# Kernel tuning notes

Hardware: AMD Instinct MI355X
Metric: run time of the kernel (lower is better)

Reference implementation:

```python
import jax, jax.numpy as jnp
import numpy as np

FRAME_LEN = 400
HOP = 160
FFT_LEN = 512
PREEMPH = 0.97
MEL_FLOOR = 1.192092955078125e-07


def _hertz_to_mel(freq):
    return 1127.0 * np.log(1.0 + freq / 700.0)


def _mel_filter_bank(num_frequency_bins=256, num_mel_filters=80, min_frequency=20.0,
                     max_frequency=8000.0, sampling_rate=16000):
    mel_min = _hertz_to_mel(min_frequency)
    mel_max = _hertz_to_mel(max_frequency)
    mel_freqs = np.linspace(mel_min, mel_max, num_mel_filters + 2)
    # NOTE: source has filter_freqs = mel_freqs (mel-space, intentional replication of bug)
    filter_freqs = mel_freqs
    fft_bin_width = sampling_rate / (num_frequency_bins * 2)
    fft_freqs = _hertz_to_mel(fft_bin_width * np.arange(num_frequency_bins))
    filter_diff = np.diff(filter_freqs)
    slopes = filter_freqs[None, :] - fft_freqs[:, None]          # [256, 82]
    down_slopes = -slopes[:, :-2] / filter_diff[:-1]
    up_slopes = slopes[:, 2:] / filter_diff[1:]
    fb = np.maximum(0.0, np.minimum(down_slopes, up_slopes))      # [256, 80]
    # F.pad(mel_filters, (0,0,0,1)) -> one extra zero row -> [257, 80]
    return np.pad(fb, ((0, 1), (0, 0))).astype(np.float32)


def _window():
    n = np.arange(FRAME_LEN)
    hann = 0.5 - 0.5 * np.cos(2.0 * np.pi * n / (FRAME_LEN - 1))  # periodic=False
    return (hann ** 0.85).astype(np.float32)


def setup_inputs() -> dict:
    key = jax.random.key(0)
    T = 9_600_000  # 10 min @ 16 kHz
    raw_speech = jax.random.normal(key, (1, T), dtype=jnp.float32)
    return {
        "raw_speech": raw_speech,
        "mel_filters": jnp.asarray(_mel_filter_bank()),  # [257, 80]
        "window": jnp.asarray(_window()),                # [400]
    }


def reference(raw_speech, mel_filters, window):
    wav = raw_speech.reshape(-1) * 32768.0  # * 2**15
    num_frames = 1 + (wav.shape[0] - FRAME_LEN) // HOP
    idx = jnp.arange(num_frames)[:, None] * HOP + jnp.arange(FRAME_LEN)[None, :]
    frames = wav[idx]                                         # [F, 400]
    frames = frames - frames.mean(axis=1, keepdims=True)      # remove DC offset
    # preemphasis: y[0] = x[0]*(1-p), y[n] = x[n] - p*x[n-1]
    pre = jnp.concatenate(
        [frames[:, :1] * (1.0 - PREEMPH), frames[:, 1:] - PREEMPH * frames[:, :-1]],
        axis=1,
    )
    pre = pre * window
    padded = jnp.pad(pre, ((0, 0), (0, FFT_LEN - FRAME_LEN)))  # [F, 512]
    spec = jnp.abs(jnp.fft.rfft(padded, axis=1)) ** 2          # [F, 257]
    mel = jnp.log(jnp.maximum(spec @ mel_filters, MEL_FLOOR))  # [F, 80]
    mean = mel.mean(axis=0, keepdims=True)
    var = mel.var(axis=0, keepdims=True, ddof=1)               # unbiased
    return (mel - mean) / jnp.sqrt(var + 1e-7)
```

## Files before the change

kernel.cpp:

```cpp
#include <hip/hip_runtime.h>
#include <math.h>

#define FRAME_LEN 400
#define HOP 160
#define NMEL 80
#define PREEMPH 0.97f
#define MEL_FLOOR 1.192092955078125e-07f
#define PPW 4
#define NSHADOW 8

#ifndef __has_builtin
#define __has_builtin(x) 0
#endif
#if __has_builtin(__builtin_amdgcn_permlane16_swap) && __has_builtin(__builtin_amdgcn_permlane32_swap)
#define USE_PLSWAP 1
#else
#define USE_PLSWAP 0
#endif
#if __has_builtin(__builtin_amdgcn_global_load_lds)
#define USE_GLL 1
typedef __attribute__((address_space(3))) void* as3_void_ptr;
typedef const __attribute__((address_space(1))) void* as1_void_cptr;
#define GLOAD_LDS(gsrc, ldst) \
    __builtin_amdgcn_global_load_lds((as1_void_cptr)(gsrc), (as3_void_ptr)(ldst), 16, 0, 0)
#else
#define USE_GLL 0
#endif

__device__ __forceinline__ float2 cadd(float2 a, float2 b){ return make_float2(a.x+b.x, a.y+b.y); }
__device__ __forceinline__ float2 csub(float2 a, float2 b){ return make_float2(a.x-b.x, a.y-b.y); }
__device__ __forceinline__ float2 cmul(float2 a, float2 b){ return make_float2(a.x*b.x-a.y*b.y, a.x*b.y+a.y*b.x); }

__device__ __forceinline__ float bperm(int addr, float v) {
    return __int_as_float(__builtin_amdgcn_ds_bpermute(addr, __float_as_int(v)));
}
template<int C>
__device__ __forceinline__ float dppf(float v) {
    return __int_as_float(__builtin_amdgcn_update_dpp(0, __float_as_int(v), C, 0xF, 0xF, false));
}
__device__ __forceinline__ float wscan_add(float v) {
    v += __int_as_float(__builtin_amdgcn_update_dpp(0, __float_as_int(v), 0x111, 0xF, 0xF, false));
    v += __int_as_float(__builtin_amdgcn_update_dpp(0, __float_as_int(v), 0x112, 0xF, 0xF, false));
    v += __int_as_float(__builtin_amdgcn_update_dpp(0, __float_as_int(v), 0x114, 0xF, 0xF, false));
    v += __int_as_float(__builtin_amdgcn_update_dpp(0, __float_as_int(v), 0x118, 0xF, 0xF, false));
    v += __int_as_float(__builtin_amdgcn_update_dpp(0, __float_as_int(v), 0x142, 0xA, 0xF, false));
    v += __int_as_float(__builtin_amdgcn_update_dpp(0, __float_as_int(v), 0x143, 0xC, 0xF, false));
    return v;
}

#if USE_PLSWAP
typedef unsigned int uint2v __attribute__((ext_vector_type(2)));
__device__ __forceinline__ void bflytw16(float2& A, float2& B, float2 tw) {
    uint2v sx = __builtin_amdgcn_permlane16_swap(__float_as_uint(A.x), __float_as_uint(B.x), false, false);
    uint2v sy = __builtin_amdgcn_permlane16_swap(__float_as_uint(A.y), __float_as_uint(B.y), false, false);
    float lx = __uint_as_float(sx.x), hx = __uint_as_float(sx.y);
    float ly = __uint_as_float(sy.x), hy = __uint_as_float(sy.y);
    float cr = tw.x * hx - tw.y * hy;
    float ci = tw.x * hy + tw.y * hx;
    float r1x = lx + cr, r2x = lx - cr;
    float r1y = ly + ci, r2y = ly - ci;
    uint2v tx = __builtin_amdgcn_permlane16_swap(__float_as_uint(r1x), __float_as_uint(r2x), false, false);
    uint2v ty = __builtin_amdgcn_permlane16_swap(__float_as_uint(r1y), __float_as_uint(r2y), false, false);
    A = make_float2(__uint_as_float(tx.x), __uint_as_float(ty.x));
    B = make_float2(__uint_as_float(tx.y), __uint_as_float(ty.y));
}
__device__ __forceinline__ void bflytw32(float2& A, float2& B, float2 tw) {
    uint2v sx = __builtin_amdgcn_permlane32_swap(__float_as_uint(A.x), __float_as_uint(B.x), false, false);
    uint2v sy = __builtin_amdgcn_permlane32_swap(__float_as_uint(A.y), __float_as_uint(B.y), false, false);
    float lx = __uint_as_float(sx.x), hx = __uint_as_float(sx.y);
    float ly = __uint_as_float(sy.x), hy = __uint_as_float(sy.y);
    float cr = tw.x * hx - tw.y * hy;
    float ci = tw.x * hy + tw.y * hx;
    float r1x = lx + cr, r2x = lx - cr;
    float r1y = ly + ci, r2y = ly - ci;
    uint2v tx = __builtin_amdgcn_permlane32_swap(__float_as_uint(r1x), __float_as_uint(r2x), false, false);
    uint2v ty = __builtin_amdgcn_permlane32_swap(__float_as_uint(r1y), __float_as_uint(r2y), false, false);
    A = make_float2(__uint_as_float(tx.x), __uint_as_float(ty.x));
    B = make_float2(__uint_as_float(tx.y), __uint_as_float(ty.y));
}
#endif

__global__ __launch_bounds__(256) void setup_kernel(const float* __restrict__ window,
                                                    float* __restrict__ frtab,
                                                    int* __restrict__ kstab,
                                                    float* __restrict__ wftab,
                                                    float* __restrict__ twtab)
{
    const int bid = blockIdx.x;
    const int t = threadIdx.x;
    if (bid == 0) {
        __shared__ float uu[256];
        const double mel_min = 1127.0 * log(1.0 + 20.0 / 700.0);
        const double mel_max = 1127.0 * log(1.0 + 8000.0 / 700.0);
        const double dstep = (mel_max - mel_min) / 81.0;
        {
            double fhz = 31.25 * (double)t;
            double m = 1127.0 * log(1.0 + fhz / 700.0);
            uu[t] = (float)((m - mel_min) / dstep);
        }
        __syncthreads();
        {
            float u = uu[t];
            frtab[t] = u - floorf(u);
        }
        if (t < 82) {
            double fhz = 700.0 * (exp((mel_min + (double)t * dstep) / 1127.0) - 1.0);
            int k = (int)ceil(fhz / 31.25);
            k = max(0, min(256, k));
            while (k > 0 && uu[k - 1] >= (float)t) --k;
            while (k < 256 && uu[k] < (float)t) ++k;
            kstab[t] = k;
        }
        if (t < 64) {
            const int l = t;
            const int bl = __brev((unsigned)l) >> 26;
            float* o = twtab + 24 * l;
            #pragma unroll
            for (int j = 1; j <= 3; ++j) {
                int d = 1 << j;
                float2 tw = make_float2(1.f, 0.f);
                if (l & d) {
                    float tt = (float)(l & (d - 1));
                    float ang = -3.1415926535897932f * tt / (float)d;
                    sincosf(ang, &tw.y, &tw.x);
                }
                o[2 * (j - 1)]     = tw.x;
                o[2 * (j - 1) + 1] = tw.y;
            }
            {
                float a16 = -3.1415926535897932f * (float)(l & 15) * (1.0f / 16.0f);
                float a32 = -3.1415926535897932f * (float)(l & 31) * (1.0f / 32.0f);
                float s16, c16, s32, c32;
                sincosf(a16, &s16, &c16);
                sincosf(a32, &s32, &c32);
                o[6] = c16; o[7] = s16; o[8] = c32; o[9] = s32;
            }
            #pragma unroll
            for (int q = 1; q < 4; ++q) {
                float ang = -6.283185307179586f * (float)(bl * q) * (1.0f / 256.0f);
                float sv, cv;
                sincosf(ang, &sv, &cv);
                o[8 + 2 * q] = cv; o[9 + 2 * q] = sv;
            }
            #pragma unroll
            for (int q = 0; q < 4; ++q) {
                int k = 4 * l + q;
                float ang = -3.1415926535897932f * (float)k * (1.0f / 256.0f);
                float sv, cv;
                sincosf(ang, &sv, &cv);
                o[16 + 2 * q] = cv; o[17 + 2 * q] = sv;
            }
        }
    } else {
        if (t >= 64) return;
        const int k = bid - 1;
        float sr = 0.f, si = 0.f;
        #pragma unroll
        for (int j = 0; j < 7; ++j) {
            int n = t + 64 * j;
            if (n < FRAME_LEN) {
                float wv = window[n] * 32768.f;
                int m = (k * n) & 511;
                float ang = -3.1415926535897932f * (float)m * (1.0f / 256.0f);
                float sv, cv;
                sincosf(ang, &sv, &cv);
                sr = fmaf(wv, cv, sr);
                si = fmaf(wv, sv, si);
            }
        }
        sr = wscan_add(sr);
        si = wscan_add(si);
        if (t == 63) { wftab[2 * k] = sr; wftab[2 * k + 1] = si; }
    }
}

__global__ __launch_bounds__(64, 8) void feat_kernel(
    const float* __restrict__ raw, const float* __restrict__ window,
    float* __restrict__ mel_out, double* __restrict__ accum,
    const float* __restrict__ frtab, const int* __restrict__ kstab,
    const float* __restrict__ wftab, const float* __restrict__ twtab, int F)
{
    __shared__ __align__(16) float wlds[FRAME_LEN];
    __shared__ __align__(16) float xu[2][560];
    __shared__ __align__(16) float pfx[2][256];

    const int l = threadIdx.x;
    const int NP = (F + 1) >> 1;
    const int basePair = blockIdx.x * PPW;

    if (basePair < NP) {
        int fA0 = 2 * basePair;
        bool hasB0 = (fA0 + 1) < F;
        const float* g = raw + (size_t)fA0 * HOP;
#if USE_GLL
        GLOAD_LDS(g + 4 * l, xu[0]);
        if (hasB0 || l < 36) GLOAD_LDS(g + 256 + 4 * l, xu[0] + 256);
        if (hasB0 && l < 12) GLOAD_LDS(g + 512 + 4 * l, xu[0] + 512);
#else
        float4 a = ((const float4*)g)[l];
        float4 b = make_float4(0.f,0.f,0.f,0.f);
        float4 c = make_float4(0.f,0.f,0.f,0.f);
        if (hasB0 || l < 36) b = ((const float4*)g)[64 + l];
        if (hasB0 && l < 12) c = ((const float4*)g)[128 + l];
        ((float4*)xu[0])[l] = a;
        ((float4*)xu[0])[64 + l] = b;
        if (l < 12) ((float4*)xu[0])[128 + l] = c;
#endif
    }

    for (int i = l; i < FRAME_LEN; i += 64) wlds[i] = window[i] * 32768.f;

    const int bl   = __brev((unsigned)l) >> 26;
    const int adrX = (l ^ 63) << 2;
    const int adr0 = ((64 - l) & 63) << 2;

    float sg[4];
    #pragma unroll
    for (int j = 0; j < 4; ++j) sg[j] = (l & (1 << j)) ? -1.f : 1.f;

    float2 dt[3], tw16, tw32, w2[4], wk[4];
    {
        const float2* tl = (const float2*)(twtab + 24 * l);
        dt[0] = tl[0];
        dt[1] = tl[1];
        dt[2] = tl[2];
        tw16  = tl[3];
        tw32  = tl[4];
        w2[1] = tl[5];
        w2[2] = tl[6];
        w2[3] = tl[7];
        wk[0] = tl[8];
        wk[1] = tl[9];
        wk[2] = tl[10];
        wk[3] = tl[11];
    }
#if !USE_PLSWAP
    float2 dtf[2];
    float sgf[2];
    #pragma unroll
    for (int j = 4; j <= 5; ++j) {
        int d = 1 << j;
        sgf[j - 4] = (l & d) ? -1.f : 1.f;
        float2 tw = make_float2(1.f, 0.f);
        if (l & d) {
            float tt = (float)(l & (d - 1));
            float ang = -3.1415926535897932f * tt / (float)d;
            sincosf(ang, &tw.y, &tw.x);
        }
        dtf[j - 4] = tw;
    }
#endif

    float wfr[4], wfi[4];
    {
        const float2* wf2 = (const float2*)wftab;
        float2 w0 = wf2[4 * l], w1 = wf2[4 * l + 1], w2v = wf2[4 * l + 2], w3 = wf2[4 * l + 3];
        wfr[0] = w0.x; wfi[0] = w0.y; wfr[1] = w1.x; wfi[1] = w1.y;
        wfr[2] = w2v.x; wfi[2] = w2v.y; wfr[3] = w3.x; wfi[3] = w3.y;
    }

    float fr1[4];
    {
        float4 fv = *(const float4*)(frtab + 4 * l);
        fr1[0] = fv.x; fr1[1] = fv.y; fr1[2] = fv.z; fr1[3] = fv.w;
    }
    int a0 = kstab[l], b0 = kstab[l + 1], e0 = kstab[l + 2];
    int a1 = 1, b1 = 1, e1 = 1;
    if (l < 16) { a1 = kstab[64 + l]; b1 = kstab[65 + l]; e1 = kstab[66 + l]; }

    float acc_s0 = 0.f, acc_q0 = 0.f;
    float acc_s1 = 0.f, acc_q1 = 0.f;

    int  fPrev = -1;
    bool hasBPrev = false;
    float vA0 = 0.f, vA1 = 0.f, vB0 = 0.f, vB1 = 0.f;

    for (int fi = 0; fi < PPW; ++fi) {
        int P = basePair + fi;
        if (P >= NP) break;
        int fA = 2 * P;
        bool hasB = (fA + 1) < F;
        const int cur = fi & 1;

        asm volatile("s_waitcnt vmcnt(0)" ::: "memory");

        const bool ldn = (fi + 1 < PPW) && (P + 1 < NP);
        if (ldn) {
            int fAn = 2 * (P + 1);
            bool hasBn = (fAn + 1) < F;
            const float* g = raw + (size_t)fAn * HOP;
            float* xn = xu[cur ^ 1];
#if USE_GLL
            GLOAD_LDS(g + 4 * l, xn);
            if (hasBn || l < 36) GLOAD_LDS(g + 256 + 4 * l, xn + 256);
            if (hasBn && l < 12) GLOAD_LDS(g + 512 + 4 * l, xn + 512);
#else
            float4 a = ((const float4*)g)[l];
            float4 b = make_float4(0.f,0.f,0.f,0.f);
            float4 c = make_float4(0.f,0.f,0.f,0.f);
            if (hasBn || l < 36) b = ((const float4*)g)[64 + l];
            if (hasBn && l < 12) c = ((const float4*)g)[128 + l];
            ((float4*)xn)[l] = a;
            ((float4*)xn)[64 + l] = b;
            if (l < 12) ((float4*)xn)[128 + l] = c;
#endif
        }

        if (fPrev >= 0) {
            mel_out[(size_t)fPrev * NMEL + l] = vA0;
            if (l < 16) mel_out[(size_t)fPrev * NMEL + 64 + l] = vA1;
            if (hasBPrev) {
                mel_out[(size_t)(fPrev + 1) * NMEL + l] = vB0;
                if (l < 16) mel_out[(size_t)(fPrev + 1) * NMEL + 64 + l] = vB1;
            }
        }

        const float* xc = xu[cur];
        float2 Z[2][4];
        float smA = 0.f, smB = 0.f;
        #pragma unroll
        for (int r = 0; r < 4; ++r) {
            int off = 128 * r + 2 * bl;
            if (off < FRAME_LEN) {
                float2 xA = *(const float2*)(xc + off);
                float2 xB = *(const float2*)(xc + 160 + off);
                float xm1A = (off == 0) ? xA.x : xc[off - 1];
                float xm1B = (off == 0) ? xB.x : xc[159 + off];
                float2 wn  = *(const float2*)(wlds + off);
                smA += xA.x + xA.y;
                smB += xB.x + xB.y;
                Z[0][r] = make_float2(fmaf(-PREEMPH, xm1A, xA.x) * wn.x,
                                      fmaf(-PREEMPH, xA.x,  xA.y) * wn.y);
                Z[1][r] = make_float2(fmaf(-PREEMPH, xm1B, xB.x) * wn.x,
                                      fmaf(-PREEMPH, xB.x,  xB.y) * wn.y);
            } else {
                Z[0][r] = make_float2(0.f, 0.f);
                Z[1][r] = make_float2(0.f, 0.f);
            }
        }
        float totA = __int_as_float(__builtin_amdgcn_readlane(__float_as_int(wscan_add(smA)), 63));
        float totB = __int_as_float(__builtin_amdgcn_readlane(__float_as_int(wscan_add(smB)), 63));
        float KA = totA * (1.0f / (float)FRAME_LEN) * (1.0f - PREEMPH);
        float KB = totB * (1.0f / (float)FRAME_LEN) * (1.0f - PREEMPH);

        #pragma unroll
        for (int s = 0; s < 2; ++s) {
            float2 t0 = cadd(Z[s][0], Z[s][2]);
            float2 t1 = csub(Z[s][0], Z[s][2]);
            float2 t2 = cadd(Z[s][1], Z[s][3]);
            float2 t3 = csub(Z[s][1], Z[s][3]);
            Z[s][0] = cadd(t0, t2);
            Z[s][2] = csub(t0, t2);
            Z[s][1] = make_float2(t1.x + t3.y, t1.y - t3.x);
            Z[s][3] = make_float2(t1.x - t3.y, t1.y + t3.x);
            #pragma unroll
            for (int q = 1; q < 4; ++q) Z[s][q] = cmul(Z[s][q], w2[q]);
        }

        #pragma unroll
        for (int s = 0; s < 2; ++s)
        #pragma unroll
        for (int q = 0; q < 4; ++q) {
            float ox = dppf<0xB1>(Z[s][q].x), oy = dppf<0xB1>(Z[s][q].y);
            Z[s][q].x = fmaf(sg[0], Z[s][q].x, ox);
            Z[s][q].y = fmaf(sg[0], Z[s][q].y, oy);
        }
        #pragma unroll
        for (int s = 0; s < 2; ++s)
        #pragma unroll
        for (int q = 0; q < 4; ++q) {
            float2 Zw = cmul(Z[s][q], dt[0]);
            float ox = dppf<0x4E>(Zw.x), oy = dppf<0x4E>(Zw.y);
            Z[s][q].x = fmaf(sg[1], Zw.x, ox);
            Z[s][q].y = fmaf(sg[1], Zw.y, oy);
        }
        #pragma unroll
        for (int s = 0; s < 2; ++s)
        #pragma unroll
        for (int q = 0; q < 4; ++q) {
            float2 Zw = cmul(Z[s][q], dt[1]);
            float ox = __shfl_xor(Zw.x, 4, 64), oy = __shfl_xor(Zw.y, 4, 64);
            Z[s][q].x = fmaf(sg[2], Zw.x, ox);
            Z[s][q].y = fmaf(sg[2], Zw.y, oy);
        }
        #pragma unroll
        for (int s = 0; s < 2; ++s)
        #pragma unroll
        for (int q = 0; q < 4; ++q) {
            float2 Zw = cmul(Z[s][q], dt[2]);
            float ox = dppf<0x128>(Zw.x), oy = dppf<0x128>(Zw.y);
            Z[s][q].x = fmaf(sg[3], Zw.x, ox);
            Z[s][q].y = fmaf(sg[3], Zw.y, oy);
        }
#if USE_PLSWAP
        #pragma unroll
        for (int s = 0; s < 2; ++s) {
            bflytw16(Z[s][0], Z[s][1], tw16);
            bflytw16(Z[s][2], Z[s][3], tw16);
        }
        #pragma unroll
        for (int s = 0; s < 2; ++s) {
            bflytw32(Z[s][0], Z[s][1], tw32);
            bflytw32(Z[s][2], Z[s][3], tw32);
        }
#else
        #pragma unroll
        for (int s = 0; s < 2; ++s)
        #pragma unroll
        for (int q = 0; q < 4; ++q) {
            float2 Zw = cmul(Z[s][q], dtf[0]);
            float ox = __shfl_xor(Zw.x, 16, 64), oy = __shfl_xor(Zw.y, 16, 64);
            Z[s][q].x = fmaf(sgf[0], Zw.x, ox);
            Z[s][q].y = fmaf(sgf[0], Zw.y, oy);
        }
        #pragma unroll
        for (int s = 0; s < 2; ++s)
        #pragma unroll
        for (int q = 0; q < 4; ++q) {
            float2 Zw = cmul(Z[s][q], dtf[1]);
            float ox = __shfl_xor(Zw.x, 32, 64), oy = __shfl_xor(Zw.y, 32, 64);
            Z[s][q].x = fmaf(sgf[1], Zw.x, ox);
            Z[s][q].y = fmaf(sgf[1], Zw.y, oy);
        }
#endif

        #pragma unroll
        for (int s = 0; s < 2; ++s) {
            float Ks = (s == 0) ? KA : KB;
            float zcr[4], zci[4];
            zcr[0] = bperm(adr0, Z[s][0].x);
            zci[0] = bperm(adr0, Z[s][0].y);
            zcr[1] = bperm(adrX, Z[s][3].x);
            zci[1] = bperm(adrX, Z[s][3].y);
            zcr[2] = bperm(adrX, Z[s][2].x);
            zci[2] = bperm(adrX, Z[s][2].y);
            zcr[3] = bperm(adrX, Z[s][1].x);
            zci[3] = bperm(adrX, Z[s][1].y);

            float pw[4], pv[4];
            #pragma unroll
            for (int q = 0; q < 4; ++q) {
                float Er = 0.5f * (Z[s][q].x + zcr[q]);
                float Ei = 0.5f * (Z[s][q].y - zci[q]);
                float Or = 0.5f * (Z[s][q].y + zci[q]);
                float Oi = 0.5f * (zcr[q] - Z[s][q].x);
                float Xr = Er + Or * wk[q].x - Oi * wk[q].y;
                float Xi = Ei + Or * wk[q].y + Oi * wk[q].x;
                Xr = fmaf(-Ks, wfr[q], Xr);
                Xi = fmaf(-Ks, wfi[q], Xi);
                pw[q] = Xr * Xr + Xi * Xi;
                pv[q] = pw[q] * fr1[q];
            }
            float A0 = pw[0], A1 = A0 + pw[1], A2 = A1 + pw[2], A3 = A2 + pw[3];
            float B0 = pv[0], B1 = B0 + pv[1], B2 = B1 + pv[2], B3 = B2 + pv[3];
            float sA = wscan_add(A3);
            float sB = wscan_add(B3);
            float exA = sA - A3;
            float exB = sB - B3;
            float* pP = pfx[0];
            float* pF = pfx[1];
            ((float4*)pP)[l] = make_float4(exA + A0, exA + A1, exA + A2, exA + A3);
            ((float4*)pF)[l] = make_float4(exB + B0, exB + B1, exB + B2, exB + B3);

            bool act = (s == 0) || hasB;
            if (act) {
                float E1a = pF[a0 - 1], E1b = pF[b0 - 1], E1e = pF[e0 - 1];
                float EAb = pP[b0 - 1], EAe = pP[e0 - 1];
                float acc = fmaf(2.f, E1b, -E1a) - E1e + (EAe - EAb);
                float v = __logf(fmaxf(acc, MEL_FLOOR));
                if (s == 0) vA0 = v; else vB0 = v;
                acc_s0 += v; acc_q0 = fmaf(v, v, acc_q0);
                if (l < 16) {
                    float F1a = pF[a1 - 1], F1b = pF[b1 - 1], F1e = pF[e1 - 1];
                    float FAb = pP[b1 - 1], FAe = pP[e1 - 1];
                    float ac2 = fmaf(2.f, F1b, -F1a) - F1e + (FAe - FAb);
                    float v1 = __logf(fmaxf(ac2, MEL_FLOOR));
                    if (s == 0) vA1 = v1; else vB1 = v1;
                    acc_s1 += v1; acc_q1 = fmaf(v1, v1, acc_q1);
                }
            }
        }
        fPrev = fA;
        hasBPrev = hasB;
    }

    if (fPrev >= 0) {
        mel_out[(size_t)fPrev * NMEL + l] = vA0;
        if (l < 16) mel_out[(size_t)fPrev * NMEL + 64 + l] = vA1;
        if (hasBPrev) {
            mel_out[(size_t)(fPrev + 1) * NMEL + l] = vB0;
            if (l < 16) mel_out[(size_t)(fPrev + 1) * NMEL + 64 + l] = vB1;
        }
    }

    double* A = accum + (blockIdx.x & (NSHADOW - 1)) * 160;
    atomicAdd(&A[l], (double)acc_s0);
    atomicAdd(&A[80 + l], (double)acc_q0);
    if (l < 16) {
        atomicAdd(&A[64 + l], (double)acc_s1);
        atomicAdd(&A[144 + l], (double)acc_q1);
    }
}

__global__ __launch_bounds__(256) void norm_kernel(
    float* __restrict__ mel, const double* __restrict__ accum, int F)
{
    __shared__ float s_mean[NMEL], s_inv[NMEL];
    int t = threadIdx.x;
    if (t < NMEL) {
        double S = 0.0, Q = 0.0;
        #pragma unroll
        for (int j = 0; j < NSHADOW; ++j) {
            S += accum[j * 160 + t];
            Q += accum[j * 160 + 80 + t];
        }
        double mean = S / (double)F;
        double var = (Q - S * S / (double)F) / (double)(F - 1);
        s_mean[t] = (float)mean;
        s_inv[t]  = (float)(1.0 / sqrt(var + 1e-7));
    }
    __syncthreads();
    unsigned n = (unsigned)F * NMEL;
    unsigned stride = gridDim.x * 256u * 4u;
    unsigned i = (blockIdx.x * 256u + (unsigned)t) * 4u;
    int c = (int)(i % NMEL);
    float m0 = s_mean[c],     r0 = s_inv[c];
    float m1 = s_mean[c + 1], r1 = s_inv[c + 1];
    float m2 = s_mean[c + 2], r2 = s_inv[c + 2];
    float m3 = s_mean[c + 3], r3 = s_inv[c + 3];
    for (; i < n; i += stride) {
        float4 v = *(float4*)(mel + i);
        v.x = (v.x - m0) * r0;
        v.y = (v.y - m1) * r1;
        v.z = (v.z - m2) * r2;
        v.w = (v.w - m3) * r3;
        *(float4*)(mel + i) = v;
    }
}

extern "C" void kernel_launch(void* const* d_in, const int* in_sizes, int n_in,
                              void* d_out, int out_size, void* d_ws, size_t ws_size,
                              hipStream_t stream)
{
    const float* raw = (const float*)d_in[0];
    const float* window = (const float*)d_in[2];
    float* out = (float*)d_out;

    int N = in_sizes[0];
    int F = 1 + (N - FRAME_LEN) / HOP;

    double* accum = (double*)d_ws;
    float*  frtab = (float*)((char*)d_ws + NSHADOW * 160 * sizeof(double));
    int*    kstab = (int*)((char*)d_ws + 11264);
    float*  wftab = (float*)((char*)d_ws + 11776);
    float*  twtab = (float*)((char*)d_ws + 13824);

    hipMemsetAsync(d_ws, 0, NSHADOW * 160 * sizeof(double), stream);
    setup_kernel<<<257, 256, 0, stream>>>(window, frtab, kstab, wftab, twtab);
    int NP = (F + 1) / 2;
    int gridA = (NP + PPW - 1) / PPW;
    feat_kernel<<<gridA, 64, 0, stream>>>(raw, window, out, accum, frtab, kstab, wftab, twtab, F);
    norm_kernel<<<2560, 256, 0, stream>>>(out, accum, F);
}
```

Baseline: 141.4 us.

## Fold accumulator zeroing into setup, simplify FFT stage and raise frames per wave

Removes the separate memset launch by zeroing the double accumulators inside the setup kernel. It replaces the radix-4 twiddle multiply in one FFT stage with a lane-conditional swap and negate. It also drops the 0.5 scaling in the real-FFT post-processing, compensating by doubling the DC correction constant, scaling the mel floor by 4 and subtracting ln 4 after the log. Frames per wave go from 4 to 12, which cuts grid size and amortizes per-wave setup but lowers parallelism.

```diff
diff --git a/kernel.cpp b/kernel.cpp
--- a/kernel.cpp
+++ b/kernel.cpp
@@ -5,8 +5,9 @@
 #define HOP 160
 #define NMEL 80
 #define PREEMPH 0.97f
-#define MEL_FLOOR 1.192092955078125e-07f
-#define PPW 4
+#define MEL_FLOOR4 4.7683718203125e-07f
+#define LN4 1.3862943611198906f
+#define PPW 12
 #define NSHADOW 8
 
 #ifndef __has_builtin
@@ -84,12 +85,15 @@
                                                     float* __restrict__ frtab,
                                                     int* __restrict__ kstab,
                                                     float* __restrict__ wftab,
-                                                    float* __restrict__ twtab)
+                                                    float* __restrict__ twtab,
+                                                    double* __restrict__ accum)
 {
     const int bid = blockIdx.x;
     const int t = threadIdx.x;
     if (bid == 0) {
         __shared__ float uu[256];
+        #pragma unroll
+        for (int j = 0; j < 5; ++j) accum[t + 256 * j] = 0.0;
         const double mel_min = 1127.0 * log(1.0 + 20.0 / 700.0);
         const double mel_max = 1127.0 * log(1.0 + 8000.0 / 700.0);
         const double dstep = (mel_max - mel_min) / 81.0;
@@ -217,13 +221,14 @@
     float sg[4];
     #pragma unroll
     for (int j = 0; j < 4; ++j) sg[j] = (l & (1 << j)) ? -1.f : 1.f;
-
-    float2 dt[3], tw16, tw32, w2[4], wk[4];
+    const bool m2 = ((l & 3) == 3);
+    const float s2f = m2 ? -1.f : 1.f;
+
+    float2 dt4, dt8, tw16, tw32, w2[4], wk[4];
     {
         const float2* tl = (const float2*)(twtab + 24 * l);
-        dt[0] = tl[0];
-        dt[1] = tl[1];
-        dt[2] = tl[2];
+        dt4   = tl[1];
+        dt8   = tl[2];
         tw16  = tl[3];
         tw32  = tl[4];
         w2[1] = tl[5];
@@ -340,8 +345,9 @@
         }
         float totA = __int_as_float(__builtin_amdgcn_readlane(__float_as_int(wscan_add(smA)), 63));
         float totB = __int_as_float(__builtin_amdgcn_readlane(__float_as_int(wscan_add(smB)), 63));
-        float KA = totA * (1.0f / (float)FRAME_LEN) * (1.0f - PREEMPH);
-        float KB = totB * (1.0f / (float)FRAME_LEN) * (1.0f - PREEMPH);
+        const float KC2 = (2.0f / (float)FRAME_LEN) * (1.0f - PREEMPH);
+        float KA = totA * KC2;
+        float KB = totB * KC2;
 
         #pragma unroll
         for (int s = 0; s < 2; ++s) {
@@ -369,16 +375,18 @@
         for (int s = 0; s < 2; ++s)
         #pragma unroll
         for (int q = 0; q < 4; ++q) {
-            float2 Zw = cmul(Z[s][q], dt[0]);
-            float ox = dppf<0x4E>(Zw.x), oy = dppf<0x4E>(Zw.y);
-            Z[s][q].x = fmaf(sg[1], Zw.x, ox);
-            Z[s][q].y = fmaf(sg[1], Zw.y, oy);
+            float zx = Z[s][q].x, zy = Z[s][q].y;
+            float wx = m2 ? zy : zx;
+            float wy = (m2 ? zx : zy) * s2f;
+            float ox = dppf<0x4E>(wx), oy = dppf<0x4E>(wy);
+            Z[s][q].x = fmaf(sg[1], wx, ox);
+            Z[s][q].y = fmaf(sg[1], wy, oy);
         }
         #pragma unroll
         for (int s = 0; s < 2; ++s)
         #pragma unroll
         for (int q = 0; q < 4; ++q) {
-            float2 Zw = cmul(Z[s][q], dt[1]);
+            float2 Zw = cmul(Z[s][q], dt4);
             float ox = __shfl_xor(Zw.x, 4, 64), oy = __shfl_xor(Zw.y, 4, 64);
             Z[s][q].x = fmaf(sg[2], Zw.x, ox);
             Z[s][q].y = fmaf(sg[2], Zw.y, oy);
@@ -387,7 +395,7 @@
         for (int s = 0; s < 2; ++s)
         #pragma unroll
         for (int q = 0; q < 4; ++q) {
-            float2 Zw = cmul(Z[s][q], dt[2]);
+            float2 Zw = cmul(Z[s][q], dt8);
             float ox = dppf<0x128>(Zw.x), oy = dppf<0x128>(Zw.y);
             Z[s][q].x = fmaf(sg[3], Zw.x, ox);
             Z[s][q].y = fmaf(sg[3], Zw.y, oy);
@@ -440,10 +448,10 @@
             float pw[4], pv[4];
             #pragma unroll
             for (int q = 0; q < 4; ++q) {
-                float Er = 0.5f * (Z[s][q].x + zcr[q]);
-                float Ei = 0.5f * (Z[s][q].y - zci[q]);
-                float Or = 0.5f * (Z[s][q].y + zci[q]);
-                float Oi = 0.5f * (zcr[q] - Z[s][q].x);
+                float Er = Z[s][q].x + zcr[q];
+                float Ei = Z[s][q].y - zci[q];
+                float Or = Z[s][q].y + zci[q];
+                float Oi = zcr[q] - Z[s][q].x;
                 float Xr = Er + Or * wk[q].x - Oi * wk[q].y;
                 float Xi = Ei + Or * wk[q].y + Oi * wk[q].x;
                 Xr = fmaf(-Ks, wfr[q], Xr);
@@ -467,14 +475,14 @@
                 float E1a = pF[a0 - 1], E1b = pF[b0 - 1], E1e = pF[e0 - 1];
                 float EAb = pP[b0 - 1], EAe = pP[e0 - 1];
                 float acc = fmaf(2.f, E1b, -E1a) - E1e + (EAe - EAb);
-                float v = __logf(fmaxf(acc, MEL_FLOOR));
+                float v = __logf(fmaxf(acc, MEL_FLOOR4)) - LN4;
                 if (s == 0) vA0 = v; else vB0 = v;
                 acc_s0 += v; acc_q0 = fmaf(v, v, acc_q0);
                 if (l < 16) {
                     float F1a = pF[a1 - 1], F1b = pF[b1 - 1], F1e = pF[e1 - 1];
                     float FAb = pP[b1 - 1], FAe = pP[e1 - 1];
                     float ac2 = fmaf(2.f, F1b, -F1a) - F1e + (FAe - FAb);
-                    float v1 = __logf(fmaxf(ac2, MEL_FLOOR));
+                    float v1 = __logf(fmaxf(ac2, MEL_FLOOR4)) - LN4;
                     if (s == 0) vA1 = v1; else vB1 = v1;
                     acc_s1 += v1; acc_q1 = fmaf(v1, v1, acc_q1);
                 }
@@ -555,8 +563,7 @@
     float*  wftab = (float*)((char*)d_ws + 11776);
     float*  twtab = (float*)((char*)d_ws + 13824);
 
-    hipMemsetAsync(d_ws, 0, NSHADOW * 160 * sizeof(double), stream);
-    setup_kernel<<<257, 256, 0, stream>>>(window, frtab, kstab, wftab, twtab);
+    setup_kernel<<<257, 256, 0, stream>>>(window, frtab, kstab, wftab, twtab, accum);
     int NP = (F + 1) / 2;
     int gridA = (NP + PPW - 1) / PPW;
     feat_kernel<<<gridA, 64, 0, stream>>>(raw, window, out, accum, frtab, kstab, wftab, twtab, F);
```

Result: slower. 147.4 us (+4.3%).
